# Performance work log

Hardware: AMD Instinct MI355X
Metric: run time of the kernel (lower is better)

Reference implementation:

```python
import jax, jax.numpy as jnp
import numpy as np

B, IN, OUT = 8192, 4096, 4096

def setup_inputs() -> dict:
    key = jax.random.key(0)
    k1, k2, k3 = jax.random.split(key, 3)
    x = jax.random.normal(k1, (B, IN), dtype=jnp.float32)
    # nn.Linear default init: U(-1/sqrt(in), 1/sqrt(in))
    bound = 1.0 / np.sqrt(IN)
    W = jax.random.uniform(k2, (OUT, IN), dtype=jnp.float32, minval=-bound, maxval=bound)
    b = jax.random.uniform(k3, (OUT,), dtype=jnp.float32, minval=-bound, maxval=bound)
    return {"x": x, "W": W, "b": b}

def reference(x, W, b):
    # L2-normalize each row (eps added to norm, matching torch)
    norm = jnp.sqrt(jnp.sum(x * x, axis=1, keepdims=True))
    x_n = x / (norm + 1e-8)
    # Linear: y = x_n @ W^T + b, then ReLU
    y = jnp.einsum('bi,oi->bo', x_n, W) + b
    return jax.nn.relu(y)
```

## Files before the change

kernel.cpp:

```cpp
#include <hip/hip_runtime.h>
#include <hip/hip_bf16.h>
#include <cstdint>
#include <cstddef>

#define GLB(p)  ((const __attribute__((address_space(1))) void*)(p))
#define LDSP(p) ((__attribute__((address_space(3))) void*)(p))

typedef __attribute__((ext_vector_type(8))) __bf16 bf16x8;
typedef __attribute__((ext_vector_type(4))) float  f32x4;
typedef __attribute__((ext_vector_type(8))) unsigned short u16x8;

static constexpr int Mdim = 8192, Ndim = 4096, Kdim = 4096;

#define S_BAR()      do { asm volatile("" ::: "memory"); __builtin_amdgcn_s_barrier(); asm volatile("" ::: "memory"); } while (0)
#define WAIT_LGKM(n) asm volatile("s_waitcnt lgkmcnt(" #n ")" ::: "memory")
#define WAIT_VM(n)   asm volatile("s_waitcnt vmcnt(" #n ")" ::: "memory")

static __device__ __forceinline__ unsigned short f2bf_bits(float f) {
    __hip_bfloat16 h = __float2bfloat16(f);
    return __builtin_bit_cast(unsigned short, h);
}

static __device__ __forceinline__ int swz16k(int p) {
    return p ^ (((p >> 7) & 7) << 4);
}

__global__ void __launch_bounds__(256) preproc_kernel(const float* __restrict__ x,
                                                      const float* __restrict__ Wf,
                                                      __hip_bfloat16* __restrict__ xn,
                                                      __hip_bfloat16* __restrict__ Wb)
{
    const int row = blockIdx.x;
    const int t = threadIdx.x;

    const float4* xr = (const float4*)(x + (size_t)row * Kdim);
    float4 v[4];
    float s = 0.f;
#pragma unroll
    for (int i = 0; i < 4; ++i) {
        v[i] = xr[i * 256 + t];
        s += v[i].x * v[i].x + v[i].y * v[i].y + v[i].z * v[i].z + v[i].w * v[i].w;
    }
#pragma unroll
    for (int off = 32; off > 0; off >>= 1) s += __shfl_down(s, off, 64);
    __shared__ float red[4];
    const int lane = t & 63, w = t >> 6;
    if (lane == 0) red[w] = s;
    __syncthreads();
    const float tot = red[0] + red[1] + red[2] + red[3];
    const float inv = 1.f / (sqrtf(tot) + 1e-8f);
    ushort4* xo = (ushort4*)(xn + (size_t)row * Kdim);
#pragma unroll
    for (int i = 0; i < 4; ++i) {
        ushort4 o;
        o.x = f2bf_bits(v[i].x * inv);
        o.y = f2bf_bits(v[i].y * inv);
        o.z = f2bf_bits(v[i].z * inv);
        o.w = f2bf_bits(v[i].w * inv);
        xo[i * 256 + t] = o;
    }

    const size_t idx = (size_t)row * 256 + t;
    const float4* p = (const float4*)Wf + idx * 2;
    const float4 a = p[0], c = p[1];
    u16x8 o;
    o[0] = f2bf_bits(a.x); o[1] = f2bf_bits(a.y);
    o[2] = f2bf_bits(a.z); o[3] = f2bf_bits(a.w);
    o[4] = f2bf_bits(c.x); o[5] = f2bf_bits(c.y);
    o[6] = f2bf_bits(c.z); o[7] = f2bf_bits(c.w);
    *((u16x8*)Wb + idx) = o;
}

__global__ void __launch_bounds__(512, 2) gemm256_8p(
        const __hip_bfloat16* __restrict__ A,
        const __hip_bfloat16* __restrict__ B,
        const float* __restrict__ bias,
        float* __restrict__ out)
{
    constexpr int NT  = Kdim / 64;
    constexpr int NTN = Ndim / 256;
    constexpr int NWG = (Mdim / 256) * NTN;
    extern __shared__ char smem[];

    const int bid = blockIdx.x;
    const int swz = (bid & 7) * (NWG / 8) + (bid >> 3);
    const int m0 = (swz / NTN) * 256;
    const int n0 = (swz % NTN) * 256;

    const int tid  = threadIdx.x;
    const int lane = tid & 63;
    const int w    = tid >> 6;
    const int wm   = w >> 2;
    const int wn   = w & 3;
    const int fr   = lane & 15;
    const int ko2  = (lane >> 4) * 16;
    const int xm   = (lane & 7) << 4;
    const int brow = (wn & 1) * 64;

    const int p0 = tid * 16;
    const int p1 = 8192 + tid * 16;
    const int q0 = swz16k(p0);
    const int q1 = swz16k(p1);
    const int sr0 = q0 >> 7, sc0 = (q0 & 127) >> 1;
    const int sr1 = q1 >> 7, sc1 = (q1 & 127) >> 1;

    const __hip_bfloat16* Ab0 = A + (size_t)(m0 + sr0) * Kdim + sc0;
    const __hip_bfloat16* Ab1 = A + (size_t)(m0 + sr1) * Kdim + sc1;
    const __hip_bfloat16* Bb0 = B + (size_t)(n0 + sr0) * Kdim + sc0;
    const __hip_bfloat16* Bb1 = B + (size_t)(n0 + sr1) * Kdim + sc1;

#define STAGE_A(tt, h) do { \
        char* ld_ = smem + ((2 * (tt) + (h)) & 3) * 16384; \
        __builtin_amdgcn_global_load_lds(GLB(Ab0 + (size_t)(h) * (128 * Kdim) + (tt) * 64), LDSP(ld_ + p0), 16, 0, 0); \
        __builtin_amdgcn_global_load_lds(GLB(Ab1 + (size_t)(h) * (128 * Kdim) + (tt) * 64), LDSP(ld_ + p1), 16, 0, 0); \
    } while (0)
#define STAGE_B(tt, h) do { \
        char* ld_ = smem + 65536 + ((2 * (tt) + (h)) & 3) * 16384; \
        __builtin_amdgcn_global_load_lds(GLB(Bb0 + (size_t)(h) * (128 * Kdim) + (tt) * 64), LDSP(ld_ + p0), 16, 0, 0); \
        __builtin_amdgcn_global_load_lds(GLB(Bb1 + (size_t)(h) * (128 * Kdim) + (tt) * 64), LDSP(ld_ + p1), 16, 0, 0); \
    } while (0)

#define LDS_RD(base, row, kb) (*(const bf16x8*)(smem + ((((base) + (row) * 128 + (kb))) ^ xm)))

    f32x4 acc[8][4];
#pragma unroll
    for (int i = 0; i < 8; ++i)
#pragma unroll
        for (int j = 0; j < 4; ++j) acc[i][j] = (f32x4){0.f, 0.f, 0.f, 0.f};

    bf16x8 afr[4][2], bfr[2][2];

    STAGE_A(0, 0); STAGE_A(0, 1); STAGE_B(0, 0); STAGE_B(0, 1);
    STAGE_A(1, 0); STAGE_A(1, 1);
    WAIT_VM(4);
    S_BAR();

#pragma unroll 2
    for (int t = 0; t < NT; ++t) {
        const int sa = ((2 * t + wm) & 3) * 16384;
        const int sb = 65536 + ((2 * t + (wn >> 1)) & 3) * 16384;
        const int tb = (t + 1) & (NT - 1);
        const int ta = (t + 2) & (NT - 1);

#pragma unroll
        for (int i = 0; i < 4; ++i) {
            afr[i][0] = LDS_RD(sa, i * 16 + fr, ko2);
            afr[i][1] = LDS_RD(sa, i * 16 + fr, 64 + ko2);
        }
#pragma unroll
        for (int j = 0; j < 2; ++j) {
            bfr[j][0] = LDS_RD(sb, brow + j * 16 + fr, ko2);
            bfr[j][1] = LDS_RD(sb, brow + j * 16 + fr, 64 + ko2);
        }
        STAGE_B(tb, 0);
        WAIT_LGKM(8);
        S_BAR();
        WAIT_LGKM(0);
        __builtin_amdgcn_sched_barrier(0);
        __builtin_amdgcn_s_setprio(1);
#pragma unroll
        for (int i = 0; i < 4; ++i)
#pragma unroll
            for (int j = 0; j < 2; ++j) {
                acc[i][j] = __builtin_amdgcn_mfma_f32_16x16x32_bf16(afr[i][0], bfr[j][0], acc[i][j], 0, 0, 0);
                acc[i][j] = __builtin_amdgcn_mfma_f32_16x16x32_bf16(afr[i][1], bfr[j][1], acc[i][j], 0, 0, 0);
            }
        __builtin_amdgcn_s_setprio(0);
        S_BAR();

#pragma unroll
        for (int j = 0; j < 2; ++j) {
            bfr[j][0] = LDS_RD(sb, brow + (2 + j) * 16 + fr, ko2);
            bfr[j][1] = LDS_RD(sb, brow + (2 + j) * 16 + fr, 64 + ko2);
        }
        STAGE_B(tb, 1);
        S_BAR();
        WAIT_LGKM(0);
        __builtin_amdgcn_sched_barrier(0);
        __builtin_amdgcn_s_setprio(1);
#pragma unroll
        for (int i = 0; i < 4; ++i)
#pragma unroll
            for (int j = 0; j < 2; ++j) {
                acc[i][2 + j] = __builtin_amdgcn_mfma_f32_16x16x32_bf16(afr[i][0], bfr[j][0], acc[i][2 + j], 0, 0, 0);
                acc[i][2 + j] = __builtin_amdgcn_mfma_f32_16x16x32_bf16(afr[i][1], bfr[j][1], acc[i][2 + j], 0, 0, 0);
            }
        __builtin_amdgcn_s_setprio(0);
        S_BAR();

#pragma unroll
        for (int i = 0; i < 4; ++i) {
            afr[i][0] = LDS_RD(sa, (4 + i) * 16 + fr, ko2);
            afr[i][1] = LDS_RD(sa, (4 + i) * 16 + fr, 64 + ko2);
        }
        S_BAR();
        WAIT_LGKM(0);
        __builtin_amdgcn_sched_barrier(0);
        __builtin_amdgcn_s_setprio(1);
#pragma unroll
        for (int i = 0; i < 4; ++i)
#pragma unroll
            for (int j = 0; j < 2; ++j) {
                acc[4 + i][2 + j] = __builtin_amdgcn_mfma_f32_16x16x32_bf16(afr[i][0], bfr[j][0], acc[4 + i][2 + j], 0, 0, 0);
                acc[4 + i][2 + j] = __builtin_amdgcn_mfma_f32_16x16x32_bf16(afr[i][1], bfr[j][1], acc[4 + i][2 + j], 0, 0, 0);
            }
        __builtin_amdgcn_s_setprio(0);
        S_BAR();

#pragma unroll
        for (int j = 0; j < 2; ++j) {
            bfr[j][0] = LDS_RD(sb, brow + j * 16 + fr, ko2);
            bfr[j][1] = LDS_RD(sb, brow + j * 16 + fr, 64 + ko2);
        }
        STAGE_A(ta, 0); STAGE_A(ta, 1);
        S_BAR();
        WAIT_LGKM(0);
        __builtin_amdgcn_sched_barrier(0);
        __builtin_amdgcn_s_setprio(1);
#pragma unroll
        for (int i = 0; i < 4; ++i)
#pragma unroll
            for (int j = 0; j < 2; ++j) {
                acc[4 + i][j] = __builtin_amdgcn_mfma_f32_16x16x32_bf16(afr[i][0], bfr[j][0], acc[4 + i][j], 0, 0, 0);
                acc[4 + i][j] = __builtin_amdgcn_mfma_f32_16x16x32_bf16(afr[i][1], bfr[j][1], acc[4 + i][j], 0, 0, 0);
            }
        __builtin_amdgcn_s_setprio(0);
        WAIT_VM(4);
        S_BAR();
    }
    WAIT_VM(0);

#undef STAGE_A
#undef STAGE_B
#undef LDS_RD

    const int cl = lane & 15;
    const int rl = (lane >> 4) * 4;
#pragma unroll
    for (int j = 0; j < 4; ++j) {
        const int col = n0 + wn * 64 + j * 16 + cl;
        const float bv = bias[col];
#pragma unroll
        for (int i = 0; i < 8; ++i) {
            const int row = m0 + wm * 128 + i * 16 + rl;
            float* po = out + (size_t)row * Ndim + col;
#pragma unroll
            for (int q = 0; q < 4; ++q) {
                const float r = acc[i][j][q] + bv;
                po[(size_t)q * Ndim] = r > 0.f ? r : 0.f;
            }
        }
    }
}

__global__ void __launch_bounds__(256) gemm_bias_relu_kernel(
        const __hip_bfloat16* __restrict__ A,
        const __hip_bfloat16* __restrict__ B,
        const float* __restrict__ bias,
        float* __restrict__ out)
{
    constexpr int BM = 128, BN = 128, BK = 32;
    constexpr int NT_N = Ndim / BN;
    constexpr int NWG  = (Mdim / BM) * NT_N;

    __shared__ __bf16 As[BM * BK];
    __shared__ __bf16 Bs[BN * BK];

    const int bid = blockIdx.x;
    const int swz = (bid & 7) * (NWG / 8) + (bid >> 3);
    const int by = swz / NT_N, bx = swz % NT_N;
    const int m0 = by * BM, n0 = bx * BN;

    const int tid  = threadIdx.x;
    const int lane = tid & 63;
    const int w    = tid >> 6;
    const int wm   = w >> 1, wn = w & 1;

    const int o0 = w * 1024 + lane * 16;
    const int o1 = o0 + 4096;
    const int r0 = o0 >> 6, e0 = (o0 & 63) >> 1;
    const int r1 = o1 >> 6, e1 = (o1 & 63) >> 1;

    const __hip_bfloat16* a0 = A + (size_t)(m0 + r0) * Kdim + e0;
    const __hip_bfloat16* a1 = A + (size_t)(m0 + r1) * Kdim + e1;
    const __hip_bfloat16* b0 = B + (size_t)(n0 + r0) * Kdim + e0;
    const __hip_bfloat16* b1 = B + (size_t)(n0 + r1) * Kdim + e1;
    __bf16* lA0 = As + (o0 >> 1);
    __bf16* lA1 = As + (o1 >> 1);
    __bf16* lB0 = Bs + (o0 >> 1);
    __bf16* lB1 = Bs + (o1 >> 1);

    f32x4 acc[4][4];
#pragma unroll
    for (int i = 0; i < 4; ++i)
#pragma unroll
        for (int j = 0; j < 4; ++j) acc[i][j] = (f32x4){0.f, 0.f, 0.f, 0.f};

    const int fr = lane & 15;
    const int ko = (lane >> 4) * 8;

    for (int kt = 0; kt < Kdim; kt += BK) {
        __builtin_amdgcn_global_load_lds(GLB(a0 + kt), LDSP(lA0), 16, 0, 0);
        __builtin_amdgcn_global_load_lds(GLB(a1 + kt), LDSP(lA1), 16, 0, 0);
        __builtin_amdgcn_global_load_lds(GLB(b0 + kt), LDSP(lB0), 16, 0, 0);
        __builtin_amdgcn_global_load_lds(GLB(b1 + kt), LDSP(lB1), 16, 0, 0);
        __syncthreads();

        bf16x8 af[4], bfr[4];
#pragma unroll
        for (int i = 0; i < 4; ++i)
            af[i]  = *(const bf16x8*)&As[(wm * 64 + i * 16 + fr) * BK + ko];
#pragma unroll
        for (int j = 0; j < 4; ++j)
            bfr[j] = *(const bf16x8*)&Bs[(wn * 64 + j * 16 + fr) * BK + ko];

#pragma unroll
        for (int i = 0; i < 4; ++i)
#pragma unroll
            for (int j = 0; j < 4; ++j)
                acc[i][j] = __builtin_amdgcn_mfma_f32_16x16x32_bf16(af[i], bfr[j], acc[i][j], 0, 0, 0);
        __syncthreads();
    }

    const int cl = lane & 15;
    const int rl = (lane >> 4) * 4;
#pragma unroll
    for (int j = 0; j < 4; ++j) {
        const int col = n0 + wn * 64 + j * 16 + cl;
        const float bv = bias[col];
#pragma unroll
        for (int i = 0; i < 4; ++i) {
            const int row = m0 + wm * 64 + i * 16 + rl;
            float* po = out + (size_t)row * Ndim + col;
#pragma unroll
            for (int q = 0; q < 4; ++q) {
                const float r = acc[i][j][q] + bv;
                po[(size_t)q * Ndim] = r > 0.f ? r : 0.f;
            }
        }
    }
}

__global__ void __launch_bounds__(256) rownorm_only_kernel(const float* __restrict__ x,
                                                           float* __restrict__ invn)
{
    const int row = blockIdx.x;
    const int t = threadIdx.x;
    const float4* xr = (const float4*)(x + (size_t)row * Kdim);
    float s = 0.f;
#pragma unroll
    for (int i = 0; i < 4; ++i) {
        const float4 v = xr[i * 256 + t];
        s += v.x * v.x + v.y * v.y + v.z * v.z + v.w * v.w;
    }
#pragma unroll
    for (int off = 32; off > 0; off >>= 1) s += __shfl_down(s, off, 64);
    __shared__ float red[4];
    if ((t & 63) == 0) red[t >> 6] = s;
    __syncthreads();
    if (t == 0) {
        const float tot = red[0] + red[1] + red[2] + red[3];
        invn[row] = 1.f / (sqrtf(tot) + 1e-8f);
    }
}

__global__ void __launch_bounds__(256) fallback_gemm_kernel(
        const float* __restrict__ x, const float* __restrict__ W,
        const float* __restrict__ b, const float* __restrict__ invn,
        float* __restrict__ out)
{
    __shared__ float At[16][17], Bt[16][17];
    const int tx = threadIdx.x & 15, ty = threadIdx.x >> 4;
    const int m = blockIdx.y * 16 + ty;
    const int n = blockIdx.x * 16 + tx;
    float s = 0.f;
    for (int k0 = 0; k0 < Kdim; k0 += 16) {
        At[ty][tx] = x[(size_t)m * Kdim + k0 + tx];
        Bt[ty][tx] = W[(size_t)(blockIdx.x * 16 + ty) * Kdim + k0 + tx];
        __syncthreads();
#pragma unroll
        for (int kk = 0; kk < 16; ++kk) s += At[ty][kk] * Bt[tx][kk];
        __syncthreads();
    }
    s = s * invn[m] + b[n];
    out[(size_t)m * Ndim + n] = s > 0.f ? s : 0.f;
}

extern "C" void kernel_launch(void* const* d_in, const int* in_sizes, int n_in,
                              void* d_out, int out_size, void* d_ws, size_t ws_size,
                              hipStream_t stream)
{
    (void)in_sizes; (void)n_in; (void)out_size;
    const float* x = (const float*)d_in[0];
    const float* W = (const float*)d_in[1];
    const float* b = (const float*)d_in[2];
    float* out = (float*)d_out;

    const size_t needA = (size_t)Mdim * Kdim * sizeof(__hip_bfloat16);
    const size_t needW = (size_t)Ndim * Kdim * sizeof(__hip_bfloat16);

    if (ws_size >= needA + needW) {
        __hip_bfloat16* Xn = (__hip_bfloat16*)d_ws;
        __hip_bfloat16* Wb = (__hip_bfloat16*)((char*)d_ws + needA);
        preproc_kernel<<<Mdim, 256, 0, stream>>>(x, W, Xn, Wb);

        hipError_t e = hipFuncSetAttribute((const void*)gemm256_8p,
                                           hipFuncAttributeMaxDynamicSharedMemorySize,
                                           131072);
        if (e == hipSuccess) {
            gemm256_8p<<<(Mdim / 256) * (Ndim / 256), 512, 131072, stream>>>(Xn, Wb, b, out);
        } else {
            gemm_bias_relu_kernel<<<(Mdim / 128) * (Ndim / 128), 256, 0, stream>>>(Xn, Wb, b, out);
        }
    } else {
        float* invn = (float*)d_ws;
        rownorm_only_kernel<<<Mdim, 256, 0, stream>>>(x, invn);
        dim3 g(Ndim / 16, Mdim / 16);
        fallback_gemm_kernel<<<g, 256, 0, stream>>>(x, W, b, invn, out);
    }
}
```

Before: 292.2 us.

## Restructure GEMM main loop to hold all B fragments and stream A in four phases

The inner loop now loads all four B fragment columns once per K-tile and streams A fragments two rows at a time across four MFMA phases. The per-phase block barriers and sched_barriers of the old 4-phase ping-pong are dropped; one barrier per iteration remains before the A restage. This is meant to cut synchronisation overhead and let the compiler overlap LDS reads with MFMAs. The tradeoff is less explicit control over instruction ordering and possible LDS hazards, since B is restaged into slots that other waves may still be reading. Register pressure also shifts between the A and B fragment arrays.

```diff
diff --git a/kernel.cpp b/kernel.cpp
--- a/kernel.cpp
+++ b/kernel.cpp
@@ -122,13 +122,26 @@
 
 #define LDS_RD(base, row, kb) (*(const bf16x8*)(smem + ((((base) + (row) * 128 + (kb))) ^ xm)))
 
+#define A_READS(mb) do { \
+    _Pragma("unroll") for (int i = 0; i < 2; ++i) { \
+        afr[i][0] = LDS_RD(sa, ((mb) + i) * 16 + fr, ko2); \
+        afr[i][1] = LDS_RD(sa, ((mb) + i) * 16 + fr, 64 + ko2); } } while (0)
+
+#define MFMA_PHASE(mb) do { \
+    __builtin_amdgcn_s_setprio(1); \
+    _Pragma("unroll") for (int kk = 0; kk < 2; ++kk) \
+    _Pragma("unroll") for (int i = 0; i < 2; ++i) \
+    _Pragma("unroll") for (int j = 0; j < 4; ++j) \
+        acc[(mb) + i][j] = __builtin_amdgcn_mfma_f32_16x16x32_bf16(afr[i][kk], bfr[j][kk], acc[(mb) + i][j], 0, 0, 0); \
+    __builtin_amdgcn_s_setprio(0); } while (0)
+
     f32x4 acc[8][4];
 #pragma unroll
     for (int i = 0; i < 8; ++i)
 #pragma unroll
         for (int j = 0; j < 4; ++j) acc[i][j] = (f32x4){0.f, 0.f, 0.f, 0.f};
 
-    bf16x8 afr[4][2], bfr[2][2];
+    bf16x8 afr[2][2], bfr[4][2];
 
     STAGE_A(0, 0); STAGE_A(0, 1); STAGE_B(0, 0); STAGE_B(0, 1);
     STAGE_A(1, 0); STAGE_A(1, 1);
@@ -143,88 +156,25 @@
         const int ta = (t + 2) & (NT - 1);
 
 #pragma unroll
-        for (int i = 0; i < 4; ++i) {
-            afr[i][0] = LDS_RD(sa, i * 16 + fr, ko2);
-            afr[i][1] = LDS_RD(sa, i * 16 + fr, 64 + ko2);
-        }
-#pragma unroll
-        for (int j = 0; j < 2; ++j) {
+        for (int j = 0; j < 4; ++j) {
             bfr[j][0] = LDS_RD(sb, brow + j * 16 + fr, ko2);
             bfr[j][1] = LDS_RD(sb, brow + j * 16 + fr, 64 + ko2);
         }
-        STAGE_B(tb, 0);
-        WAIT_LGKM(8);
+        A_READS(0);
+        STAGE_B(tb, 0); STAGE_B(tb, 1);
+        MFMA_PHASE(0);
+
+        A_READS(2);
+        MFMA_PHASE(2);
+
+        A_READS(4);
+        MFMA_PHASE(4);
+
+        A_READS(6);
+        WAIT_LGKM(0);
         S_BAR();
-        WAIT_LGKM(0);
-        __builtin_amdgcn_sched_barrier(0);
-        __builtin_amdgcn_s_setprio(1);
-#pragma unroll
-        for (int i = 0; i < 4; ++i)
-#pragma unroll
-            for (int j = 0; j < 2; ++j) {
-                acc[i][j] = __builtin_amdgcn_mfma_f32_16x16x32_bf16(afr[i][0], bfr[j][0], acc[i][j], 0, 0, 0);
-                acc[i][j] = __builtin_amdgcn_mfma_f32_16x16x32_bf16(afr[i][1], bfr[j][1], acc[i][j], 0, 0, 0);
-            }
-        __builtin_amdgcn_s_setprio(0);
-        S_BAR();
-
-#pragma unroll
-        for (int j = 0; j < 2; ++j) {
-            bfr[j][0] = LDS_RD(sb, brow + (2 + j) * 16 + fr, ko2);
-            bfr[j][1] = LDS_RD(sb, brow + (2 + j) * 16 + fr, 64 + ko2);
-        }
-        STAGE_B(tb, 1);
-        S_BAR();
-        WAIT_LGKM(0);
-        __builtin_amdgcn_sched_barrier(0);
-        __builtin_amdgcn_s_setprio(1);
-#pragma unroll
-        for (int i = 0; i < 4; ++i)
-#pragma unroll
-            for (int j = 0; j < 2; ++j) {
-                acc[i][2 + j] = __builtin_amdgcn_mfma_f32_16x16x32_bf16(afr[i][0], bfr[j][0], acc[i][2 + j], 0, 0, 0);
-                acc[i][2 + j] = __builtin_amdgcn_mfma_f32_16x16x32_bf16(afr[i][1], bfr[j][1], acc[i][2 + j], 0, 0, 0);
-            }
-        __builtin_amdgcn_s_setprio(0);
-        S_BAR();
-
-#pragma unroll
-        for (int i = 0; i < 4; ++i) {
-            afr[i][0] = LDS_RD(sa, (4 + i) * 16 + fr, ko2);
-            afr[i][1] = LDS_RD(sa, (4 + i) * 16 + fr, 64 + ko2);
-        }
-        S_BAR();
-        WAIT_LGKM(0);
-        __builtin_amdgcn_sched_barrier(0);
-        __builtin_amdgcn_s_setprio(1);
-#pragma unroll
-        for (int i = 0; i < 4; ++i)
-#pragma unroll
-            for (int j = 0; j < 2; ++j) {
-                acc[4 + i][2 + j] = __builtin_amdgcn_mfma_f32_16x16x32_bf16(afr[i][0], bfr[j][0], acc[4 + i][2 + j], 0, 0, 0);
-                acc[4 + i][2 + j] = __builtin_amdgcn_mfma_f32_16x16x32_bf16(afr[i][1], bfr[j][1], acc[4 + i][2 + j], 0, 0, 0);
-            }
-        __builtin_amdgcn_s_setprio(0);
-        S_BAR();
-
-#pragma unroll
-        for (int j = 0; j < 2; ++j) {
-            bfr[j][0] = LDS_RD(sb, brow + j * 16 + fr, ko2);
-            bfr[j][1] = LDS_RD(sb, brow + j * 16 + fr, 64 + ko2);
-        }
         STAGE_A(ta, 0); STAGE_A(ta, 1);
-        S_BAR();
-        WAIT_LGKM(0);
-        __builtin_amdgcn_sched_barrier(0);
-        __builtin_amdgcn_s_setprio(1);
-#pragma unroll
-        for (int i = 0; i < 4; ++i)
-#pragma unroll
-            for (int j = 0; j < 2; ++j) {
-                acc[4 + i][j] = __builtin_amdgcn_mfma_f32_16x16x32_bf16(afr[i][0], bfr[j][0], acc[4 + i][j], 0, 0, 0);
-                acc[4 + i][j] = __builtin_amdgcn_mfma_f32_16x16x32_bf16(afr[i][1], bfr[j][1], acc[4 + i][j], 0, 0, 0);
-            }
-        __builtin_amdgcn_s_setprio(0);
+        MFMA_PHASE(6);
         WAIT_VM(4);
         S_BAR();
     }
@@ -233,6 +183,8 @@
 #undef STAGE_A
 #undef STAGE_B
 #undef LDS_RD
+#undef A_READS
+#undef MFMA_PHASE
 
     const int cl = lane & 15;
     const int rl = (lane >> 4) * 4;
```

Result: no change. 287.3 us (-1.7%).
